# Kernel optimization log

Hardware: AMD Instinct MI355X
Metric: run time of the kernel (lower is better)

Reference implementation:

```python
import jax, jax.numpy as jnp
import numpy as np

B, S, D = 2, 2048, 2048
H, HKV, HD = 16, 2, 128
THETA = 10000.0


def setup_inputs() -> dict:
    key = jax.random.key(0)
    ks = jax.random.split(key, 5)
    x = jax.random.normal(ks[0], (B, S, D), jnp.float32)
    Wq = jax.random.normal(ks[1], (D, H * HD), jnp.float32) * 0.02
    Wk = jax.random.normal(ks[2], (D, HKV * HD), jnp.float32) * 0.02
    Wv = jax.random.normal(ks[3], (D, HKV * HD), jnp.float32) * 0.02
    Wo = jax.random.normal(ks[4], (H * HD, D), jnp.float32) * 0.02
    mask = jnp.tril(jnp.ones((S, S), jnp.int32))[None, None]  # causal [1,1,S,S]
    return {"x": x, "mask": mask, "Wq": Wq, "Wk": Wk, "Wv": Wv, "Wo": Wo}


def _rope(t, seq_len):
    # t: [B, S, H, HD]; matches RotaryPositionalEmbedding (cos/sin broadcast [S,1,HD])
    inv_freq = 1.0 / (THETA ** (jnp.arange(0, HD, 2, dtype=jnp.float32) / HD))
    pos = jnp.arange(seq_len, dtype=jnp.float32)
    freqs = jnp.einsum('i,j->ij', pos, inv_freq)          # [S, HD/2]
    emb = jnp.concatenate([freqs, freqs], axis=-1)        # [S, HD]
    cos = jnp.cos(emb)[:, None, :]
    sin = jnp.sin(emb)[:, None, :]
    x1, x2 = jnp.split(t, 2, axis=-1)
    rot = jnp.concatenate([-x2, x1], axis=-1)             # rotate_half
    return t * cos + rot * sin


def reference(x, mask, Wq, Wk, Wv, Wo):
    Bx, Sx, _ = x.shape
    q = (x @ Wq).reshape(Bx, Sx, H, HD)
    k = (x @ Wk).reshape(Bx, Sx, HKV, HD)
    v = (x @ Wv).reshape(Bx, Sx, HKV, HD)
    q = _rope(q, Sx)
    k = _rope(k, Sx)
    rep = H // HKV
    # torch .repeat along head dim == tiling (not interleaved)
    k = jnp.tile(k, (1, 1, rep, 1))  # [B, S, H, HD]
    v = jnp.tile(v, (1, 1, rep, 1))
    scale = 1.0 / np.sqrt(HD).astype(np.float32)
    scores = jnp.einsum('bqhd,bkhd->bhqk', q, k) * scale  # [B, H, S, S]
    scores = jnp.where(mask == 0, -jnp.inf, scores)
    attn = jax.nn.softmax(scores.astype(jnp.float32), axis=-1).astype(scores.dtype)
    out = jnp.einsum('bhqk,bkhd->bqhd', attn, v).reshape(Bx, Sx, H * HD)
    return out @ Wo
```

## Files before the change

kernel.cpp:

```cpp
#include <hip/hip_runtime.h>
#include <hip/hip_bf16.h>

#define S_LEN 2048
#define DMODEL 2048
#define NHEAD 16
#define NKVH 2
#define HDIM 128
#define NROW 4096
#define NQKV 2560
#define SCALE 0.08838834764831845f

using short8 = __attribute__((ext_vector_type(8))) short;
using bf16x8 = __attribute__((ext_vector_type(8))) __bf16;
using f32x4  = __attribute__((ext_vector_type(4))) float;

__device__ __forceinline__ f32x4 mfma16(short8 a, short8 b, f32x4 c) {
  return __builtin_amdgcn_mfma_f32_16x16x32_bf16(
      __builtin_bit_cast(bf16x8, a), __builtin_bit_cast(bf16x8, b), c, 0, 0, 0);
}

__device__ __forceinline__ void gload_lds16(const void* g, void* l) {
  __builtin_amdgcn_global_load_lds(
      (const __attribute__((address_space(1))) unsigned int*)g,
      (__attribute__((address_space(3))) unsigned int*)l, 16, 0, 0);
}

__device__ __forceinline__ void storeC(float* C, long idx, float v) { C[idx] = v; }
__device__ __forceinline__ void storeC(__hip_bfloat16* C, long idx, float v) {
  C[idx] = __float2bfloat16(v);
}

__device__ __forceinline__ unsigned short bf16bits(float f) {
  __hip_bfloat16 h = __float2bfloat16(f);
  return *(unsigned short*)&h;
}

__global__ void conv_x(const float* __restrict__ x, __hip_bfloat16* __restrict__ xb) {
  long i = ((long)blockIdx.x * 256 + threadIdx.x) * 4;
  float4 v = *(const float4*)(x + i);
  __hip_bfloat16 o[4];
  o[0] = __float2bfloat16(v.x); o[1] = __float2bfloat16(v.y);
  o[2] = __float2bfloat16(v.z); o[3] = __float2bfloat16(v.w);
  *(ushort4*)(xb + i) = *(const ushort4*)o;
}

__global__ void convT3(const float* __restrict__ Wq, const float* __restrict__ Wk,
                       const float* __restrict__ Wv, __hip_bfloat16* __restrict__ dst) {
  __shared__ float t[32][33];
  int nt = blockIdx.x, kt = blockIdx.y;
  int tx = threadIdx.x, ty = threadIdx.y;
  const float* src; int Ns, n0, row_off;
  if (nt < 64)      { src = Wq; Ns = 2048; n0 = nt * 32;        row_off = n0; }
  else if (nt < 72) { src = Wk; Ns = 256;  n0 = (nt - 64) * 32; row_off = 2048 + n0; }
  else              { src = Wv; Ns = 256;  n0 = (nt - 72) * 32; row_off = 2304 + n0; }
#pragma unroll
  for (int i = 0; i < 4; i++)
    t[ty + i * 8][tx] = src[(long)(kt * 32 + ty + i * 8) * Ns + n0 + tx];
  __syncthreads();
#pragma unroll
  for (int i = 0; i < 4; i++)
    dst[(long)(row_off + ty + i * 8) * 2048 + kt * 32 + tx] =
        __float2bfloat16(t[tx][ty + i * 8]);
}

__global__ void convT(const float* __restrict__ src, __hip_bfloat16* __restrict__ dst,
                      int Ns, int row_off) {
  __shared__ float t[32][33];
  int nt = blockIdx.x, kt = blockIdx.y;
  int tx = threadIdx.x, ty = threadIdx.y;
#pragma unroll
  for (int i = 0; i < 4; i++)
    t[ty + i * 8][tx] = src[(long)(kt * 32 + ty + i * 8) * Ns + nt * 32 + tx];
  __syncthreads();
#pragma unroll
  for (int i = 0; i < 4; i++)
    dst[(long)(row_off + nt * 32 + ty + i * 8) * 2048 + kt * 32 + tx] =
        __float2bfloat16(t[tx][ty + i * 8]);
}

__global__ void mk_table(float* __restrict__ cost, float* __restrict__ sint) {
  int i = blockIdx.x * 256 + threadIdx.x;
  int s = i >> 6, j = i & 63;
  double f = pow(10000.0, -(double)j / 64.0);
  double a = (double)s * f;
  cost[i] = (float)cos(a);
  sint[i] = (float)sin(a);
}

template <typename OutT>
__global__ void gemm_bt(const __hip_bfloat16* __restrict__ A,
                        const __hip_bfloat16* __restrict__ Bt,
                        OutT* __restrict__ C, int M, int N, int K) {
  __shared__ __align__(16) __hip_bfloat16 a_lds[128 * 32];
  __shared__ __align__(16) __hip_bfloat16 b_lds[128 * 32];
  const int tid = threadIdx.x;
  const int wid = tid >> 6, lane = tid & 63;
  const int nbx = gridDim.x;
  int bid = blockIdx.y * nbx + blockIdx.x;
  const int nwg = nbx * gridDim.y;
  bid = (bid & 7) * (nwg >> 3) + (bid >> 3);
  const int m0 = (bid / nbx) * 128, n0 = (bid % nbx) * 128;
  const int wr = wid >> 1, wc = wid & 1;
  const int lrow = lane & 15, lk = lane >> 4;

  const __hip_bfloat16* ag0 = A + (long)(m0 + wid * 16 + (lane >> 2)) * K + (lane & 3) * 8;
  const __hip_bfloat16* bg0 = Bt + (long)(n0 + wid * 16 + (lane >> 2)) * K + (lane & 3) * 8;
  char* al = (char*)a_lds + wid * 1024 + lane * 16;
  char* bl = (char*)b_lds + wid * 1024 + lane * 16;

  f32x4 acc[4][4] = {};

  for (int k0 = 0; k0 < K; k0 += 32) {
    gload_lds16(ag0 + k0, al);
    gload_lds16(ag0 + 64 * (long)K + k0, al + 4096);
    gload_lds16(bg0 + k0, bl);
    gload_lds16(bg0 + 64 * (long)K + k0, bl + 4096);
    __syncthreads();
    short8 af[4], bfr[4];
#pragma unroll
    for (int mi = 0; mi < 4; mi++)
      af[mi] = *(const short8*)(a_lds + (wr * 64 + mi * 16 + lrow) * 32 + lk * 8);
#pragma unroll
    for (int ni = 0; ni < 4; ni++)
      bfr[ni] = *(const short8*)(b_lds + (wc * 64 + ni * 16 + lrow) * 32 + lk * 8);
#pragma unroll
    for (int mi = 0; mi < 4; mi++)
#pragma unroll
      for (int ni = 0; ni < 4; ni++)
        acc[mi][ni] = mfma16(af[mi], bfr[ni], acc[mi][ni]);
    __syncthreads();
  }
#pragma unroll
  for (int mi = 0; mi < 4; mi++)
#pragma unroll
    for (int ni = 0; ni < 4; ni++)
#pragma unroll
      for (int r = 0; r < 4; r++) {
        long row = m0 + wr * 64 + mi * 16 + lk * 4 + r;
        long col = n0 + wc * 64 + ni * 16 + lrow;
        storeC(C, row * N + col, acc[mi][ni][r]);
      }
}

__global__ void rope_kernel(const __hip_bfloat16* __restrict__ qkv,
                            const float* __restrict__ cost, const float* __restrict__ sint,
                            __hip_bfloat16* __restrict__ q_r, __hip_bfloat16* __restrict__ k_t) {
  int tid = threadIdx.x;
  long row = (long)blockIdx.x * 4 + (tid >> 6);
  int j = tid & 63;
  int hh = (int)(row % 18);
  long bs = row / 18;
  int s = (int)(bs & (S_LEN - 1));
  int b = (int)(bs >> 11);
  const __hip_bfloat16* src = qkv + bs * NQKV;
  float c = cost[s * 64 + j], sn = sint[s * 64 + j];
  if (hh < NHEAD) {
    int col0 = hh * HDIM;
    float lo = __bfloat162float(src[col0 + j]);
    float hi = __bfloat162float(src[col0 + j + 64]);
    __hip_bfloat16* dst = q_r + ((long)(b * NHEAD + hh) * S_LEN + s) * HDIM;
    dst[j]      = __float2bfloat16((lo * c - hi * sn) * SCALE);
    dst[j + 64] = __float2bfloat16((hi * c + lo * sn) * SCALE);
  } else {
    int kvh = hh - NHEAD;
    int col0 = DMODEL + kvh * HDIM;
    float lo = __bfloat162float(src[col0 + j]);
    float hi = __bfloat162float(src[col0 + j + 64]);
    long tb = (long)(b * NKVH + kvh) * (S_LEN * HDIM) + (long)(s >> 5) * 4096 +
              (s & 15) * 8 + (j & 7);
    int cs4 = ((s >> 4) & 1) * 4;
    int lkq = ((j >> 3) & 3) * 16;
    int dch = j >> 5;
    k_t[tb + (long)((cs4 + dch) * 64 + lkq) * 8]     = __float2bfloat16(lo * c - hi * sn);
    k_t[tb + (long)((cs4 + dch + 2) * 64 + lkq) * 8] = __float2bfloat16(hi * c + lo * sn);
  }
}

__global__ void vtrans(const __hip_bfloat16* __restrict__ qkv, __hip_bfloat16* __restrict__ v_t) {
  __shared__ __hip_bfloat16 t[32][33];
  int st = blockIdx.x, dt = blockIdx.y, bk = blockIdx.z;
  int tx = threadIdx.x, ty = threadIdx.y;
#pragma unroll
  for (int i = 0; i < 4; i++)
    t[ty + i * 8][tx] = qkv[((long)(bk >> 1) * S_LEN + st * 32 + ty + i * 8) * NQKV +
                            DMODEL + NKVH * HDIM + (bk & 1) * HDIM + dt * 32 + tx];
  __syncthreads();
  long base = (long)bk * (S_LEN * HDIM) + (long)st * 4096 + (tx >> 3) * 128 + (tx & 7);
#pragma unroll
  for (int i = 0; i < 4; i++) {
    int d = dt * 32 + ty + i * 8;
    v_t[base + (long)((d >> 4) * 64 + (d & 15)) * 8] = t[tx][ty + i * 8];
  }
}

__global__ __launch_bounds__(256, 2) void attn_kernel(
    const __hip_bfloat16* __restrict__ q_r, const __hip_bfloat16* __restrict__ k_t,
    const __hip_bfloat16* __restrict__ v_t, __hip_bfloat16* __restrict__ attn_a) {
  __shared__ __align__(16) __hip_bfloat16 k_st[2][4096];
  __shared__ __align__(16) __hip_bfloat16 v_st[2][4096];
  __shared__ __align__(16) unsigned short p_lds[4][32 * 40];
  const int tid = threadIdx.x;
  const int wid = tid >> 6, lane = tid & 63;
  const int lrow = lane & 15, lk = lane >> 4;
  const int bidx = blockIdx.x;
  const int half = bidx >> 8;
  const int r5 = bidx & 255;
  const int b = r5 >> 7;
  const int kv = (r5 >> 6) & 1;
  const int hg = (r5 >> 5) & 1;
  const int j = r5 & 31;
  const int c = half ? (63 - j) : j;
  const int h = kv + 2 * (hg * 4 + wid);
  const int q0 = c * 32;
  const int nkt = c + 1;

  const __hip_bfloat16* qb = q_r + (long)(b * NHEAD + h) * S_LEN * HDIM;
  const __hip_bfloat16* kbase = k_t + (long)(b * NKVH + kv) * (S_LEN * HDIM);
  const __hip_bfloat16* vbase = v_t + (long)(b * NKVH + kv) * (S_LEN * HDIM);

  auto stage = [&](int t, int bi) {
    const __hip_bfloat16* kg = kbase + (long)t * 4096;
    const __hip_bfloat16* vg = vbase + (long)t * 4096;
    gload_lds16(kg + tid * 8,        (char*)&k_st[bi][0] + tid * 16);
    gload_lds16(kg + 2048 + tid * 8, (char*)&k_st[bi][2048] + tid * 16);
    gload_lds16(vg + tid * 8,        (char*)&v_st[bi][0] + tid * 16);
    gload_lds16(vg + 2048 + tid * 8, (char*)&v_st[bi][2048] + tid * 16);
  };

  short8 qf[2][4];
#pragma unroll
  for (int m = 0; m < 2; m++)
#pragma unroll
    for (int dc = 0; dc < 4; dc++)
      qf[m][dc] = *(const short8*)(qb + (long)(q0 + m * 16 + lrow) * HDIM + dc * 32 + lk * 8);

  f32x4 oacc[2][8] = {};
  float mrow[2] = {4.0f, 4.0f};
  float lsum[2] = {0.f, 0.f};

  stage(0, 0);
  __syncthreads();
  for (int kt = 0; kt < nkt; kt++) {
    if (kt + 1 < nkt) stage(kt + 1, (kt + 1) & 1);
    const __hip_bfloat16* ks = &k_st[kt & 1][0];
    const __hip_bfloat16* vs = &v_st[kt & 1][0];
    const int kc0 = kt * 32;
    const bool diag = (kt == nkt - 1);

    short8 kf[2][4];
#pragma unroll
    for (int cs = 0; cs < 2; cs++)
#pragma unroll
      for (int dc = 0; dc < 4; dc++)
        kf[cs][dc] = *(const short8*)(ks + ((cs * 4 + dc) * 64 + lane) * 8);
    f32x4 sacc[2][2] = {};
#pragma unroll
    for (int dc = 0; dc < 4; dc++) {
      sacc[0][0] = mfma16(kf[0][dc], qf[0][dc], sacc[0][0]);
      sacc[0][1] = mfma16(kf[1][dc], qf[0][dc], sacc[0][1]);
      sacc[1][0] = mfma16(kf[0][dc], qf[1][dc], sacc[1][0]);
      sacc[1][1] = mfma16(kf[1][dc], qf[1][dc], sacc[1][1]);
    }
#pragma unroll
    for (int m = 0; m < 2; m++) {
      float pv[8];
#pragma unroll
      for (int cs = 0; cs < 2; cs++)
#pragma unroll
        for (int r = 0; r < 4; r++) pv[cs * 4 + r] = sacc[m][cs][r];
      if (diag) {
        int qrow = q0 + m * 16 + lrow;
#pragma unroll
        for (int cs = 0; cs < 2; cs++)
#pragma unroll
          for (int r = 0; r < 4; r++)
            if (kc0 + cs * 16 + lk * 4 + r > qrow) pv[cs * 4 + r] = -3.0e38f;
      }
      float mx = fmaxf(fmaxf(fmaxf(pv[0], pv[1]), fmaxf(pv[2], pv[3])),
                       fmaxf(fmaxf(pv[4], pv[5]), fmaxf(pv[6], pv[7])));
      if (__builtin_expect(__any(mx > mrow[m] + 8.0f), 0)) {
        float mr = fmaxf(mx, __shfl_xor(mx, 16));
        mr = fmaxf(mr, __shfl_xor(mr, 32));
        float mnew = fmaxf(mrow[m], mr);
        float fr = __expf(mrow[m] - mnew);
        lsum[m] *= fr;
        mrow[m] = mnew;
#pragma unroll
        for (int r2 = 0; r2 < 4; r2++) {
          float fro = __shfl(fr, lk * 4 + r2);
#pragma unroll
          for (int d2 = 0; d2 < 8; d2++) oacc[m][d2][r2] *= fro;
        }
      }
      float pe[8];
#pragma unroll
      for (int i = 0; i < 8; i++) pe[i] = __expf(pv[i] - mrow[m]);
      lsum[m] += ((pe[0] + pe[1]) + (pe[2] + pe[3])) + ((pe[4] + pe[5]) + (pe[6] + pe[7]));
      unsigned short pk[8];
#pragma unroll
      for (int i = 0; i < 8; i++) pk[i] = bf16bits(pe[i]);
      *(ushort4*)(&p_lds[wid][(m * 16 + lrow) * 40 + lk * 4]) = *(ushort4*)&pk[0];
      *(ushort4*)(&p_lds[wid][(m * 16 + lrow) * 40 + 16 + lk * 4]) = *(ushort4*)&pk[4];
    }
    short8 pf[2];
#pragma unroll
    for (int m = 0; m < 2; m++)
      pf[m] = *(const short8*)(&p_lds[wid][(m * 16 + lrow) * 40 + lk * 8]);
#pragma unroll
    for (int d2 = 0; d2 < 8; d2++) {
      short8 vf = *(const short8*)(vs + (d2 * 64 + lane) * 8);
      oacc[0][d2] = mfma16(pf[0], vf, oacc[0][d2]);
      oacc[1][d2] = mfma16(pf[1], vf, oacc[1][d2]);
    }
    __syncthreads();
  }

#pragma unroll
  for (int m = 0; m < 2; m++) {
    float ls = lsum[m];
    ls += __shfl_xor(ls, 16);
    ls += __shfl_xor(ls, 32);
    float inv = 1.0f / ls;
#pragma unroll
    for (int r = 0; r < 4; r++) {
      float invr = __shfl(inv, lk * 4 + r);
      long row = (long)b * S_LEN + q0 + m * 16 + lk * 4 + r;
#pragma unroll
      for (int d2 = 0; d2 < 8; d2++)
        attn_a[row * DMODEL + h * HDIM + d2 * 16 + lrow] =
            __float2bfloat16(oacc[m][d2][r] * invr);
    }
  }
}

extern "C" void kernel_launch(void* const* d_in, const int* in_sizes, int n_in,
                              void* d_out, int out_size, void* d_ws, size_t ws_size,
                              hipStream_t stream) {
  const float* x  = (const float*)d_in[0];
  const float* Wq = (const float*)d_in[2];
  const float* Wk = (const float*)d_in[3];
  const float* Wv = (const float*)d_in[4];
  const float* Wo = (const float*)d_in[5];
  float* out = (float*)d_out;

  char* ws = (char*)d_ws;
  __hip_bfloat16* xb     = (__hip_bfloat16*)(ws + 0);
  __hip_bfloat16* attn_a = xb;
  __hip_bfloat16* wt1    = (__hip_bfloat16*)(ws + 16777216);
  __hip_bfloat16* wto    = (__hip_bfloat16*)(ws + 27262976);
  __hip_bfloat16* qkv    = (__hip_bfloat16*)(ws + 35651584);
  __hip_bfloat16* q_r    = (__hip_bfloat16*)(ws + 56623104);
  __hip_bfloat16* k_t    = (__hip_bfloat16*)(ws + 73400320);
  __hip_bfloat16* v_t    = (__hip_bfloat16*)(ws + 75497472);
  float* cost            = (float*)(ws + 77594624);
  float* sint            = (float*)(ws + 78118912);

  conv_x<<<8192, 256, 0, stream>>>(x, xb);
  convT3<<<dim3(80, 64), dim3(32, 8), 0, stream>>>(Wq, Wk, Wv, wt1);
  convT<<<dim3(64, 64), dim3(32, 8), 0, stream>>>(Wo, wto, 2048, 0);
  mk_table<<<512, 256, 0, stream>>>(cost, sint);

  gemm_bt<__hip_bfloat16><<<dim3(20, 32), 256, 0, stream>>>(xb, wt1, qkv, NROW, NQKV, DMODEL);

  rope_kernel<<<18432, 256, 0, stream>>>(qkv, cost, sint, q_r, k_t);
  vtrans<<<dim3(64, 4, 4), dim3(32, 8), 0, stream>>>(qkv, v_t);

  attn_kernel<<<512, 256, 0, stream>>>(q_r, k_t, v_t, attn_a);

  gemm_bt<float><<<dim3(16, 32), 256, 0, stream>>>(attn_a, wto, out, NROW, DMODEL, DMODEL);
}
```

Baseline: 215.8 us.

## Split attention into single-wave blocks reading K/V directly from global memory

The attention kernel moves from 256-thread blocks, where four heads share K/V tiles staged in LDS, to 64-thread single-wave blocks (2048 of them) that each handle one head and one query tile. Fragments are loaded straight from global memory, and the V fragments are hoisted ahead of the softmax so their latency can overlap it. This drops the block-wide barriers and LDS staging, and the smaller blocks may spread the uneven causal work more evenly across CUs. The cost is that sharing of K/V across the four heads of a group is lost, so each tile is fetched four times over and reuse now depends on cache, and register pressure rises.

```diff
diff --git a/kernel.cpp b/kernel.cpp
--- a/kernel.cpp
+++ b/kernel.cpp
@@ -193,24 +193,22 @@
   }
 }
 
-__global__ __launch_bounds__(256, 2) void attn_kernel(
+__global__ __launch_bounds__(64) void attn_kernel(
     const __hip_bfloat16* __restrict__ q_r, const __hip_bfloat16* __restrict__ k_t,
     const __hip_bfloat16* __restrict__ v_t, __hip_bfloat16* __restrict__ attn_a) {
-  __shared__ __align__(16) __hip_bfloat16 k_st[2][4096];
-  __shared__ __align__(16) __hip_bfloat16 v_st[2][4096];
-  __shared__ __align__(16) unsigned short p_lds[4][32 * 40];
-  const int tid = threadIdx.x;
-  const int wid = tid >> 6, lane = tid & 63;
+  __shared__ __align__(16) unsigned short p_lds[32 * 40];
+  const int lane = threadIdx.x;
   const int lrow = lane & 15, lk = lane >> 4;
   const int bidx = blockIdx.x;
-  const int half = bidx >> 8;
   const int r5 = bidx & 255;
-  const int b = r5 >> 7;
-  const int kv = (r5 >> 6) & 1;
-  const int hg = (r5 >> 5) & 1;
-  const int j = r5 & 31;
-  const int c = half ? (63 - j) : j;
-  const int h = kv + 2 * (hg * 4 + wid);
+  const int mm = bidx >> 8;
+  const int combo = r5 & 31;
+  const int q8 = r5 >> 5;
+  const int c = (mm < 4) ? (mm * 8 + q8) : 63 - ((mm - 4) * 8 + q8);
+  const int t = combo & 7;
+  const int kv = (combo >> 3) & 1;
+  const int b = combo >> 4;
+  const int h = kv + 2 * t;
   const int q0 = c * 32;
   const int nkt = c + 1;
 
@@ -218,15 +216,6 @@
   const __hip_bfloat16* kbase = k_t + (long)(b * NKVH + kv) * (S_LEN * HDIM);
   const __hip_bfloat16* vbase = v_t + (long)(b * NKVH + kv) * (S_LEN * HDIM);
 
-  auto stage = [&](int t, int bi) {
-    const __hip_bfloat16* kg = kbase + (long)t * 4096;
-    const __hip_bfloat16* vg = vbase + (long)t * 4096;
-    gload_lds16(kg + tid * 8,        (char*)&k_st[bi][0] + tid * 16);
-    gload_lds16(kg + 2048 + tid * 8, (char*)&k_st[bi][2048] + tid * 16);
-    gload_lds16(vg + tid * 8,        (char*)&v_st[bi][0] + tid * 16);
-    gload_lds16(vg + 2048 + tid * 8, (char*)&v_st[bi][2048] + tid * 16);
-  };
-
   short8 qf[2][4];
 #pragma unroll
   for (int m = 0; m < 2; m++)
@@ -238,12 +227,9 @@
   float mrow[2] = {4.0f, 4.0f};
   float lsum[2] = {0.f, 0.f};
 
-  stage(0, 0);
-  __syncthreads();
   for (int kt = 0; kt < nkt; kt++) {
-    if (kt + 1 < nkt) stage(kt + 1, (kt + 1) & 1);
-    const __hip_bfloat16* ks = &k_st[kt & 1][0];
-    const __hip_bfloat16* vs = &v_st[kt & 1][0];
+    const __hip_bfloat16* ks = kbase + (long)kt * 4096;
+    const __hip_bfloat16* vs = vbase + (long)kt * 4096;
     const int kc0 = kt * 32;
     const bool diag = (kt == nkt - 1);
 
@@ -261,6 +247,10 @@
       sacc[1][0] = mfma16(kf[0][dc], qf[1][dc], sacc[1][0]);
       sacc[1][1] = mfma16(kf[1][dc], qf[1][dc], sacc[1][1]);
     }
+    short8 vf[8];
+#pragma unroll
+    for (int d2 = 0; d2 < 8; d2++)
+      vf[d2] = *(const short8*)(vs + (d2 * 64 + lane) * 8);
 #pragma unroll
     for (int m = 0; m < 2; m++) {
       float pv[8];
@@ -299,20 +289,18 @@
       unsigned short pk[8];
 #pragma unroll
       for (int i = 0; i < 8; i++) pk[i] = bf16bits(pe[i]);
-      *(ushort4*)(&p_lds[wid][(m * 16 + lrow) * 40 + lk * 4]) = *(ushort4*)&pk[0];
-      *(ushort4*)(&p_lds[wid][(m * 16 + lrow) * 40 + 16 + lk * 4]) = *(ushort4*)&pk[4];
+      *(ushort4*)(&p_lds[(m * 16 + lrow) * 40 + lk * 4]) = *(ushort4*)&pk[0];
+      *(ushort4*)(&p_lds[(m * 16 + lrow) * 40 + 16 + lk * 4]) = *(ushort4*)&pk[4];
     }
     short8 pf[2];
 #pragma unroll
     for (int m = 0; m < 2; m++)
-      pf[m] = *(const short8*)(&p_lds[wid][(m * 16 + lrow) * 40 + lk * 8]);
+      pf[m] = *(const short8*)(&p_lds[(m * 16 + lrow) * 40 + lk * 8]);
 #pragma unroll
     for (int d2 = 0; d2 < 8; d2++) {
-      short8 vf = *(const short8*)(vs + (d2 * 64 + lane) * 8);
-      oacc[0][d2] = mfma16(pf[0], vf, oacc[0][d2]);
-      oacc[1][d2] = mfma16(pf[1], vf, oacc[1][d2]);
+      oacc[0][d2] = mfma16(pf[0], vf[d2], oacc[0][d2]);
+      oacc[1][d2] = mfma16(pf[1], vf[d2], oacc[1][d2]);
     }
-    __syncthreads();
   }
 
 #pragma unroll
@@ -365,7 +353,7 @@
   rope_kernel<<<18432, 256, 0, stream>>>(qkv, cost, sint, q_r, k_t);
   vtrans<<<dim3(64, 4, 4), dim3(32, 8), 0, stream>>>(qkv, v_t);
 
-  attn_kernel<<<512, 256, 0, stream>>>(q_r, k_t, v_t, attn_a);
+  attn_kernel<<<2048, 64, 0, stream>>>(q_r, k_t, v_t, attn_a);
 
   gemm_bt<float><<<dim3(16, 32), 256, 0, stream>>>(attn_a, wto, out, NROW, DMODEL, DMODEL);
 }
```

New measurement: 235.9 us. 9.3% more time.
